# Optimization experiments

Measured on AMD Instinct MI355X. Metric: run time of the kernel, lower is better.

The kernel has to match this reference:

```python
import jax, jax.numpy as jnp
import numpy as np

N_NODES = 50000
N_EDGES = 800000
IN_CH, HID, OUT_CH, HEADS = 128, 32, 32, 8
NEG_SLOPE = 0.2


def setup_inputs() -> dict:
    key = jax.random.key(0)
    ks = jax.random.split(key, 20)
    x = jax.random.normal(ks[0], (N_NODES, IN_CH), dtype=jnp.float32)
    edge_index = jax.random.randint(ks[1], (2, N_EDGES), 0, N_NODES, dtype=jnp.int64)
    s = 0.1
    # encoder layer 1: in -> hid, heads=8 (concat)
    W1 = jax.random.normal(ks[2], (IN_CH, HEADS * HID), jnp.float32) * s
    as1 = jax.random.normal(ks[3], (HEADS, HID), jnp.float32) * s
    ad1 = jax.random.normal(ks[4], (HEADS, HID), jnp.float32) * s
    b1 = jnp.zeros((HEADS * HID,), jnp.float32)
    # encoder layer 2: hid*heads -> out, heads=1
    W2 = jax.random.normal(ks[5], (HEADS * HID, OUT_CH), jnp.float32) * s
    as2 = jax.random.normal(ks[6], (1, OUT_CH), jnp.float32) * s
    ad2 = jax.random.normal(ks[7], (1, OUT_CH), jnp.float32) * s
    b2 = jnp.zeros((OUT_CH,), jnp.float32)
    # decoder layer 1: out -> hid, heads=8 (concat)
    W3 = jax.random.normal(ks[8], (OUT_CH, HEADS * HID), jnp.float32) * s
    as3 = jax.random.normal(ks[9], (HEADS, HID), jnp.float32) * s
    ad3 = jax.random.normal(ks[10], (HEADS, HID), jnp.float32) * s
    b3 = jnp.zeros((HEADS * HID,), jnp.float32)
    # decoder layer 2: hid*heads -> in, heads=1
    W4 = jax.random.normal(ks[11], (HEADS * HID, IN_CH), jnp.float32) * s
    as4 = jax.random.normal(ks[12], (1, IN_CH), jnp.float32) * s
    ad4 = jax.random.normal(ks[13], (1, IN_CH), jnp.float32) * s
    b4 = jnp.zeros((IN_CH,), jnp.float32)
    return dict(x=x, edge_index=edge_index, W1=W1, as1=as1, ad1=ad1, b1=b1,
                W2=W2, as2=as2, ad2=ad2, b2=b2, W3=W3, as3=as3, ad3=ad3, b3=b3,
                W4=W4, as4=as4, ad4=ad4, b4=b4)


def gat_conv(x, src, dst, W, a_src, a_dst, b, heads, ch):
    # PyG GATConv: h = xW, e_ij = LeakyReLU(a_src.h_j + a_dst.h_i), softmax over incoming edges of i
    h = (x @ W).reshape(-1, heads, ch)                       # [N, H, C]
    al_s = jnp.sum(h * a_src[None], axis=-1)                 # [N, H]
    al_d = jnp.sum(h * a_dst[None], axis=-1)                 # [N, H]
    e = jax.nn.leaky_relu(al_s[src] + al_d[dst], NEG_SLOPE)  # [E, H]
    emax = jax.ops.segment_max(e, dst, num_segments=N_NODES)
    ee = jnp.exp(e - emax[dst])
    denom = jax.ops.segment_sum(ee, dst, num_segments=N_NODES)
    alpha = ee / denom[dst]                                  # [E, H]
    msg = alpha[:, :, None] * h[src]                         # [E, H, C]
    out = jax.ops.segment_sum(msg, dst, num_segments=N_NODES)  # [N, H, C]
    return out.reshape(N_NODES, heads * ch) + b


def reference(x, edge_index, W1, as1, ad1, b1, W2, as2, ad2, b2,
              W3, as3, ad3, b3, W4, as4, ad4, b4):
    # add self loops (PyG default add_self_loops=True)
    loop = jnp.arange(N_NODES, dtype=edge_index.dtype)
    src = jnp.concatenate([edge_index[0], loop])
    dst = jnp.concatenate([edge_index[1], loop])
    # encode
    z = gat_conv(x, src, dst, W1, as1, ad1, b1, HEADS, HID)
    z = jax.nn.relu(z)
    z = gat_conv(z, src, dst, W2, as2, ad2, b2, 1, OUT_CH)
    # decode
    r = gat_conv(z, src, dst, W3, as3, ad3, b3, HEADS, HID)
    r = jax.nn.relu(r)
    r = gat_conv(r, src, dst, W4, as4, ad4, b4, 1, IN_CH)
    return r
```

## Files before the change

kernel.cpp:

```cpp
#include <hip/hip_runtime.h>
#include <math.h>

#define N_NODES 50000
#define N_EDGES 800000
#define N_TOT   850000
#define NSB     ((N_NODES + 255) / 256)

typedef __attribute__((ext_vector_type(8))) short short8;
typedef __attribute__((ext_vector_type(4))) float floatx4;

__device__ __forceinline__ unsigned int pack_bf16x2(float a, float b) {
    unsigned ua = __float_as_uint(a);
    unsigned ub = __float_as_uint(b);
    ua += 0x7fff + ((ua >> 16) & 1);
    ub += 0x7fff + ((ub >> 16) & 1);
    return (ua >> 16) | (ub & 0xffff0000u);
}
__device__ __forceinline__ unsigned short pack_bf16(float a) {
    unsigned ua = __float_as_uint(a);
    ua += 0x7fff + ((ua >> 16) & 1);
    return (unsigned short)(ua >> 16);
}
__device__ __forceinline__ float bf16_lo(unsigned u) { return __uint_as_float(u << 16); }
__device__ __forceinline__ float bf16_hi(unsigned u) { return __uint_as_float(u & 0xffff0000u); }

__global__ void zero_int_kernel(int* p, int n) {
    int i = blockIdx.x * blockDim.x + threadIdx.x;
    if (i < n) p[i] = 0;
}

__global__ void deg_hist_kernel(const int* __restrict__ ei, int* __restrict__ deg) {
    int e = blockIdx.x * blockDim.x + threadIdx.x;
    if (e >= N_TOT) return;
    int dst = (e < N_EDGES) ? ei[N_EDGES + e] : (e - N_EDGES);
    atomicAdd(&deg[dst], 1);
}

__global__ void block_scan_kernel(const int* __restrict__ deg, int* __restrict__ part,
                                  int* __restrict__ bsum) {
    __shared__ int tmp[256];
    int t = threadIdx.x;
    int i = blockIdx.x * 256 + t;
    int v = (i < N_NODES) ? deg[i] : 0;
    tmp[t] = v;
    __syncthreads();
    for (int d = 1; d < 256; d <<= 1) {
        int u = (t >= d) ? tmp[t - d] : 0;
        __syncthreads();
        tmp[t] += u;
        __syncthreads();
    }
    if (i < N_NODES) part[i] = tmp[t] - v;
    if (t == 255) bsum[blockIdx.x] = tmp[255];
}

__global__ void scan_bsum_kernel(int* __restrict__ bsum) {
    __shared__ int tmp[256];
    int t = threadIdx.x;
    int v = (t < NSB) ? bsum[t] : 0;
    tmp[t] = v;
    __syncthreads();
    for (int d = 1; d < 256; d <<= 1) {
        int u = (t >= d) ? tmp[t - d] : 0;
        __syncthreads();
        tmp[t] += u;
        __syncthreads();
    }
    if (t < NSB) bsum[t] = tmp[t] - v;
}

__global__ void finalize_off_kernel(const int* __restrict__ part, const int* __restrict__ bsum,
                                    int* __restrict__ off, int* __restrict__ cursor) {
    int i = blockIdx.x * 256 + threadIdx.x;
    if (i < N_NODES) {
        int o = part[i] + bsum[blockIdx.x];
        off[i] = o;
        cursor[i] = o;
    }
    if (i == 0) off[N_NODES] = N_TOT;
}

__global__ void fill_csr_kernel(const int* __restrict__ ei, int* __restrict__ cursor,
                                int* __restrict__ csr_src) {
    int e = blockIdx.x * blockDim.x + threadIdx.x;
    if (e >= N_TOT) return;
    int src, dst;
    if (e < N_EDGES) { src = ei[e]; dst = ei[N_EDGES + e]; }
    else             { src = dst = e - N_EDGES; }
    int pos = atomicAdd(&cursor[dst], 1);
    csr_src[pos] = src;
}

__global__ void wconv_kernel(const float* __restrict__ W1, const float* __restrict__ W2,
                             const float* __restrict__ W3, const float* __restrict__ W4,
                             unsigned short* __restrict__ T1, unsigned short* __restrict__ T2,
                             unsigned short* __restrict__ T3, unsigned short* __restrict__ T4) {
    int i = blockIdx.x * 256 + threadIdx.x;
    const float* W; unsigned short* T; int K, N, idx;
    if      (i < 32768) { W = W1; T = T1; K = 128; N = 256; idx = i; }
    else if (i < 40960) { W = W2; T = T2; K = 256; N = 32;  idx = i - 32768; }
    else if (i < 49152) { W = W3; T = T3; K = 32;  N = 256; idx = i - 40960; }
    else if (i < 81920) { W = W4; T = T4; K = 256; N = 128; idx = i - 49152; }
    else return;
    int n = idx / K, k = idx % K;
    T[idx] = pack_bf16(W[(size_t)k * N + n]);
}

template<int Cin, int Cout, int H, int C, int NPB, int NW_N, bool IN_BF16>
__global__ void gemm_mfma_kernel(const void* __restrict__ xin,
                                 const unsigned short* __restrict__ Wt,
                                 const float* __restrict__ a_src, const float* __restrict__ a_dst,
                                 unsigned short* __restrict__ hb,
                                 float* __restrict__ al_s, float* __restrict__ al_d) {
    constexpr int NW_M = 4 / NW_N;
    constexpr int MT_W = (NPB / 16) / NW_M;
    constexpr int NT_W = (Cout / 16) / NW_N;
    constexpr int AS   = Cin + 8;
    constexpr int SP   = Cout + 4;
    __shared__ unsigned short xs[NPB * AS];
    __shared__ float hs[NPB * SP];
    int tid = threadIdx.x;
    int n0  = blockIdx.x * NPB;

    if (IN_BF16) {
        for (int i = tid; i < NPB * Cin / 8; i += 256) {
            int n = i / (Cin / 8), k8 = i % (Cin / 8);
            uint4 q = make_uint4(0u, 0u, 0u, 0u);
            if (n0 + n < N_NODES)
                q = ((const uint4*)((const unsigned short*)xin + (size_t)(n0 + n) * Cin))[k8];
            *(uint4*)(xs + n * AS + k8 * 8) = q;
        }
    } else {
        for (int i = tid; i < NPB * Cin / 4; i += 256) {
            int n = i / (Cin / 4), k4 = i % (Cin / 4);
            float4 v = make_float4(0.f, 0.f, 0.f, 0.f);
            if (n0 + n < N_NODES)
                v = ((const float4*)((const float*)xin + (size_t)(n0 + n) * Cin))[k4];
            uint2 p;
            p.x = pack_bf16x2(v.x, v.y);
            p.y = pack_bf16x2(v.z, v.w);
            *(uint2*)(xs + n * AS + k4 * 4) = p;
        }
    }
    __syncthreads();

    int w = tid >> 6, lane = tid & 63;
    int q = lane >> 4, l16 = lane & 15;
    int wm = w / NW_N, wn = w % NW_N;
    int mbase = wm * MT_W * 16;
    int nbase = wn * NT_W * 16;

    floatx4 acc[MT_W][NT_W];
#pragma unroll
    for (int mt = 0; mt < MT_W; mt++)
#pragma unroll
        for (int nt = 0; nt < NT_W; nt++) acc[mt][nt] = (floatx4){0.f, 0.f, 0.f, 0.f};

#pragma unroll
    for (int k0 = 0; k0 < Cin; k0 += 32) {
        short8 a[MT_W], b[NT_W];
#pragma unroll
        for (int mt = 0; mt < MT_W; mt++)
            a[mt] = *(const short8*)(xs + (mbase + mt * 16 + l16) * AS + k0 + q * 8);
#pragma unroll
        for (int nt = 0; nt < NT_W; nt++)
            b[nt] = *(const short8*)(Wt + (size_t)(nbase + nt * 16 + l16) * Cin + k0 + q * 8);
#pragma unroll
        for (int mt = 0; mt < MT_W; mt++)
#pragma unroll
            for (int nt = 0; nt < NT_W; nt++)
                acc[mt][nt] = __builtin_amdgcn_mfma_f32_16x16x32_bf16(a[mt], b[nt], acc[mt][nt], 0, 0, 0);
    }

#pragma unroll
    for (int mt = 0; mt < MT_W; mt++)
#pragma unroll
        for (int nt = 0; nt < NT_W; nt++)
#pragma unroll
            for (int r = 0; r < 4; r++) {
                int nl = mbase + mt * 16 + q * 4 + r;
                int ch = nbase + nt * 16 + l16;
                hs[nl * SP + ch] = acc[mt][nt][r];
            }
    __syncthreads();

    constexpr int TPN = Cout / 32;
    constexpr int TPH = (C > 32) ? (C / 32) : 1;
    if (tid < NPB * TPN) {
        int node = tid / TPN, sub = tid % TPN;
        int gn = n0 + node;
        int head = (sub * 32) / C;
        int coff = (sub * 32) % C;
        const float* hrow = hs + node * SP + sub * 32;
        const float* ap = a_src + head * C + coff;
        const float* dp = a_dst + head * C + coff;
        float ps = 0.f, pd = 0.f;
        unsigned pk[8];
#pragma unroll
        for (int c4 = 0; c4 < 8; c4++) {
            float4 hv = *(const float4*)(hrow + c4 * 4);
            float4 av = *(const float4*)(ap + c4 * 4);
            float4 dv = *(const float4*)(dp + c4 * 4);
            ps += hv.x * av.x + hv.y * av.y + hv.z * av.z + hv.w * av.w;
            pd += hv.x * dv.x + hv.y * dv.y + hv.z * dv.z + hv.w * dv.w;
            pk[c4] = pack_bf16x2(hv.x, hv.y) | 0u;
            pk[c4] = pack_bf16x2(hv.x, hv.y);
        }
        uint4 o0, o1;
        {
            float4 h0 = *(const float4*)(hrow + 0);
            float4 h1 = *(const float4*)(hrow + 4);
            float4 h2 = *(const float4*)(hrow + 8);
            float4 h3 = *(const float4*)(hrow + 12);
            o0.x = pack_bf16x2(h0.x, h0.y); o0.y = pack_bf16x2(h0.z, h0.w);
            o0.z = pack_bf16x2(h1.x, h1.y); o0.w = pack_bf16x2(h1.z, h1.w);
            o1.x = pack_bf16x2(h2.x, h2.y); o1.y = pack_bf16x2(h2.z, h2.w);
            o1.z = pack_bf16x2(h3.x, h3.y); o1.w = pack_bf16x2(h3.z, h3.w);
        }
        uint4 o2, o3;
        {
            float4 h0 = *(const float4*)(hrow + 16);
            float4 h1 = *(const float4*)(hrow + 20);
            float4 h2 = *(const float4*)(hrow + 24);
            float4 h3 = *(const float4*)(hrow + 28);
            o2.x = pack_bf16x2(h0.x, h0.y); o2.y = pack_bf16x2(h0.z, h0.w);
            o2.z = pack_bf16x2(h1.x, h1.y); o2.w = pack_bf16x2(h1.z, h1.w);
            o3.x = pack_bf16x2(h2.x, h2.y); o3.y = pack_bf16x2(h2.z, h2.w);
            o3.z = pack_bf16x2(h3.x, h3.y); o3.w = pack_bf16x2(h3.z, h3.w);
        }
        if (gn < N_NODES) {
            uint2* dst = (uint2*)(hb + (size_t)gn * Cout + sub * 32);
            dst[0] = make_uint2(o0.x, o0.y); dst[1] = make_uint2(o0.z, o0.w);
            dst[2] = make_uint2(o1.x, o1.y); dst[3] = make_uint2(o1.z, o1.w);
            dst[4] = make_uint2(o2.x, o2.y); dst[5] = make_uint2(o2.z, o2.w);
            dst[6] = make_uint2(o3.x, o3.y); dst[7] = make_uint2(o3.z, o3.w);
        }
        if (TPH > 1) {
#pragma unroll
            for (int k = 1; k < TPH; k <<= 1) {
                ps += __shfl_xor(ps, k, 64);
                pd += __shfl_xor(pd, k, 64);
            }
            if ((sub % TPH) == 0 && gn < N_NODES) {
                al_s[gn * H + head] = ps;
                al_d[gn * H + head] = pd;
            }
        } else {
            if (gn < N_NODES) {
                al_s[gn * H + head] = ps;
                al_d[gn * H + head] = pd;
            }
        }
    }
}

template<int H, int C, bool RELU, bool OUT_BF16>
__launch_bounds__(256, 8)
__global__ void gat_agg_kernel(const unsigned short* __restrict__ hb,
                               const float* __restrict__ al_s,
                               const float* __restrict__ al_d, const int* __restrict__ off,
                               const int* __restrict__ csr_src, const float* __restrict__ bias,
                               void* __restrict__ out) {
    constexpr int HC  = H * C;
    constexpr int G   = HC / 4;
    constexpr int SUB = G / H;
    constexpr int NPW = 64 / G;
    constexpr int NPB = 4 * NPW;

    int tid  = threadIdx.x;
    int wid  = tid >> 6;
    int lane = tid & 63;
    int gi   = lane / G;
    int g    = lane % G;
    int node = blockIdx.x * NPB + wid * NPW + gi;
    if (node >= N_NODES) return;

    int head = g / SUB;
    int es   = g % SUB;
    int r0 = off[node], r1 = off[node + 1];
    float ald = al_d[node * H + head];

    float m = -INFINITY, s = 0.f;
    for (int j = r0 + es; j < r1; j += SUB) {
        int src = csr_src[j];
        float e = al_s[src * H + head] + ald;
        e = (e > 0.f) ? e : 0.2f * e;
        float M = fmaxf(m, e);
        s = s * __expf(m - M) + __expf(e - M);
        m = M;
    }
#pragma unroll
    for (int k = 1; k < SUB; k <<= 1) {
        float om = __shfl_xor(m, k, 64);
        float os = __shfl_xor(s, k, 64);
        float M = fmaxf(m, om);
        float S;
        if (M == -INFINITY) S = 0.f;
        else S = s * __expf(m - M) + os * __expf(om - M);
        m = M; s = S;
    }
    float inv_s = 1.f / s;

    const uint2* hb2 = (const uint2*)hb;
    float4 acc = ((const float4*)bias)[g];
    int j0 = r0;
    for (; j0 + 8 <= r1; j0 += 8) {
        int srcs[8];
#pragma unroll
        for (int u = 0; u < 8; u++) srcs[u] = csr_src[j0 + u];
#pragma unroll
        for (int u = 0; u < 8; u++) {
            float e = al_s[srcs[u] * H + head] + ald;
            e = (e > 0.f) ? e : 0.2f * e;
            float we = __expf(e - m) * inv_s;
            uint2 q = hb2[(size_t)srcs[u] * (HC / 4) + g];
            acc.x += we * bf16_lo(q.x); acc.y += we * bf16_hi(q.x);
            acc.z += we * bf16_lo(q.y); acc.w += we * bf16_hi(q.y);
        }
    }
    for (; j0 < r1; j0++) {
        int src = csr_src[j0];
        float e = al_s[src * H + head] + ald;
        e = (e > 0.f) ? e : 0.2f * e;
        float we = __expf(e - m) * inv_s;
        uint2 q = hb2[(size_t)src * (HC / 4) + g];
        acc.x += we * bf16_lo(q.x); acc.y += we * bf16_hi(q.x);
        acc.z += we * bf16_lo(q.y); acc.w += we * bf16_hi(q.y);
    }
    if (RELU) {
        acc.x = fmaxf(acc.x, 0.f); acc.y = fmaxf(acc.y, 0.f);
        acc.z = fmaxf(acc.z, 0.f); acc.w = fmaxf(acc.w, 0.f);
    }
    if (OUT_BF16) {
        uint2 p;
        p.x = pack_bf16x2(acc.x, acc.y);
        p.y = pack_bf16x2(acc.z, acc.w);
        ((uint2*)out)[(size_t)node * (HC / 4) + g] = p;
    } else {
        ((float4*)out)[(size_t)node * (HC / 4) + g] = acc;
    }
}

extern "C" void kernel_launch(void* const* d_in, const int* in_sizes, int n_in,
                              void* d_out, int out_size, void* d_ws, size_t ws_size,
                              hipStream_t stream) {
    const float* x   = (const float*)d_in[0];
    const int*   ei  = (const int*)d_in[1];
    const float* W1  = (const float*)d_in[2];
    const float* as1 = (const float*)d_in[3];
    const float* ad1 = (const float*)d_in[4];
    const float* b1  = (const float*)d_in[5];
    const float* W2  = (const float*)d_in[6];
    const float* as2 = (const float*)d_in[7];
    const float* ad2 = (const float*)d_in[8];
    const float* b2  = (const float*)d_in[9];
    const float* W3  = (const float*)d_in[10];
    const float* as3 = (const float*)d_in[11];
    const float* ad3 = (const float*)d_in[12];
    const float* b3  = (const float*)d_in[13];
    const float* W4  = (const float*)d_in[14];
    const float* as4 = (const float*)d_in[15];
    const float* ad4 = (const float*)d_in[16];
    const float* b4  = (const float*)d_in[17];

    char* ws = (char*)d_ws;
    size_t o = 0;
    auto alloc = [&](size_t bytes) -> void* {
        void* p = ws + o;
        o = (o + bytes + 255) & ~(size_t)255;
        return p;
    };
    unsigned short* feat_a  = (unsigned short*)alloc((size_t)N_NODES * 256 * 2);
    unsigned short* feat_b  = (unsigned short*)alloc((size_t)N_NODES * 32 * 2);
    unsigned short* h_buf   = (unsigned short*)alloc((size_t)N_NODES * 256 * 2);
    float*          al_s    = (float*)alloc((size_t)N_NODES * 8 * 4);
    float*          al_d    = (float*)alloc((size_t)N_NODES * 8 * 4);
    int*            deg     = (int*)alloc((size_t)(N_NODES + 1) * 4);
    int*            off     = (int*)alloc((size_t)(N_NODES + 1) * 4);
    int*            cursor  = (int*)alloc((size_t)N_NODES * 4);
    int*            part    = (int*)alloc((size_t)N_NODES * 4);
    int*            bsum    = (int*)alloc((size_t)256 * 4);
    int*            csr_src = (int*)alloc((size_t)N_TOT * 4);
    unsigned short* w1t     = (unsigned short*)alloc(32768 * 2);
    unsigned short* w2t     = (unsigned short*)alloc(8192 * 2);
    unsigned short* w3t     = (unsigned short*)alloc(8192 * 2);
    unsigned short* w4t     = (unsigned short*)alloc(32768 * 2);

    const int TPB = 256;
    int nb_nodes = (N_NODES + TPB - 1) / TPB;
    int nb_edges = (N_TOT + TPB - 1) / TPB;

    zero_int_kernel<<<nb_nodes, TPB, 0, stream>>>(deg, N_NODES);
    wconv_kernel<<<320, TPB, 0, stream>>>(W1, W2, W3, W4, w1t, w2t, w3t, w4t);
    deg_hist_kernel<<<nb_edges, TPB, 0, stream>>>(ei, deg);
    block_scan_kernel<<<NSB, TPB, 0, stream>>>(deg, part, bsum);
    scan_bsum_kernel<<<1, TPB, 0, stream>>>(bsum);
    finalize_off_kernel<<<NSB, TPB, 0, stream>>>(part, bsum, off, cursor);
    fill_csr_kernel<<<nb_edges, TPB, 0, stream>>>(ei, cursor, csr_src);

    auto agg_blocks = [](int hc) { return (N_NODES * (hc / 4) + 255) / 256; };

    gemm_mfma_kernel<128, 256, 8, 32, 32, 4, false>
        <<<(N_NODES + 31) / 32, TPB, 0, stream>>>(x, w1t, as1, ad1, h_buf, al_s, al_d);
    gat_agg_kernel<8, 32, true, true><<<agg_blocks(256), TPB, 0, stream>>>(h_buf, al_s, al_d, off, csr_src, b1, feat_a);

    gemm_mfma_kernel<256, 32, 1, 32, 64, 2, true>
        <<<(N_NODES + 63) / 64, TPB, 0, stream>>>(feat_a, w2t, as2, ad2, h_buf, al_s, al_d);
    gat_agg_kernel<1, 32, false, true><<<agg_blocks(32), TPB, 0, stream>>>(h_buf, al_s, al_d, off, csr_src, b2, feat_b);

    gemm_mfma_kernel<32, 256, 8, 32, 32, 4, true>
        <<<(N_NODES + 31) / 32, TPB, 0, stream>>>(feat_b, w3t, as3, ad3, h_buf, al_s, al_d);
    gat_agg_kernel<8, 32, true, true><<<agg_blocks(256), TPB, 0, stream>>>(h_buf, al_s, al_d, off, csr_src, b3, feat_a);

    gemm_mfma_kernel<256, 128, 1, 128, 32, 4, true>
        <<<(N_NODES + 31) / 32, TPB, 0, stream>>>(feat_a, w4t, as4, ad4, h_buf, al_s, al_d);
    gat_agg_kernel<1, 128, false, false><<<agg_blocks(128), TPB, 0, stream>>>(h_buf, al_s, al_d, off, csr_src, b4, d_out);
}
```

Before: 541.9 us.

## Widen aggregation gathers to 16 bytes and stage GEMM output as bf16 in shared memory

The aggregation kernel now has each thread handle 8 channels and load them with 16-byte uint4 gathers instead of 8-byte uint2, which halves the thread count per node and the number of gather instructions. The GEMM epilogue packs accumulators to bf16 straight into a shared buffer that aliases the input tile, cutting LDS use and allowing higher occupancy. Attention logits are now computed from the bf16-rounded values, which slightly changes numerics. Fewer threads per node in aggregation also lowers the parallelism available to hide gather latency.

```diff
diff --git a/kernel.cpp b/kernel.cpp
--- a/kernel.cpp
+++ b/kernel.cpp
@@ -116,9 +116,11 @@
     constexpr int MT_W = (NPB / 16) / NW_M;
     constexpr int NT_W = (Cout / 16) / NW_N;
     constexpr int AS   = Cin + 8;
-    constexpr int SP   = Cout + 4;
-    __shared__ unsigned short xs[NPB * AS];
-    __shared__ float hs[NPB * SP];
+    constexpr int HS   = Cout + 8;
+    constexpr size_t SMEM_EL = (size_t)NPB * ((AS > HS) ? AS : HS);
+    __shared__ uint4 smem_raw[(SMEM_EL * 2 + 15) / 16];
+    unsigned short* xs  = (unsigned short*)smem_raw;
+    unsigned short* hsb = (unsigned short*)smem_raw;
     int tid = threadIdx.x;
     int n0  = blockIdx.x * NPB;
 
@@ -171,6 +173,7 @@
             for (int nt = 0; nt < NT_W; nt++)
                 acc[mt][nt] = __builtin_amdgcn_mfma_f32_16x16x32_bf16(a[mt], b[nt], acc[mt][nt], 0, 0, 0);
     }
+    __syncthreads();
 
 #pragma unroll
     for (int mt = 0; mt < MT_W; mt++)
@@ -180,60 +183,41 @@
             for (int r = 0; r < 4; r++) {
                 int nl = mbase + mt * 16 + q * 4 + r;
                 int ch = nbase + nt * 16 + l16;
-                hs[nl * SP + ch] = acc[mt][nt][r];
+                hsb[nl * HS + ch] = pack_bf16(acc[mt][nt][r]);
             }
     __syncthreads();
 
-    constexpr int TPN = Cout / 32;
-    constexpr int TPH = (C > 32) ? (C / 32) : 1;
-    if (tid < NPB * TPN) {
-        int node = tid / TPN, sub = tid % TPN;
-        int gn = n0 + node;
-        int head = (sub * 32) / C;
-        int coff = (sub * 32) % C;
-        const float* hrow = hs + node * SP + sub * 32;
-        const float* ap = a_src + head * C + coff;
-        const float* dp = a_dst + head * C + coff;
+    constexpr int TPN = Cout / 16;
+    constexpr int TPH = C / 16;
+    for (int t = tid; t < NPB * TPN; t += 256) {
+        int nodeL = t / TPN, sub = t % TPN;
+        int gn = n0 + nodeL;
+        uint4 qv = *(const uint4*)(hsb + nodeL * HS + sub * 16);
+        int head = (sub * 16) / C;
+        int coff = (sub * 16) % C;
+        const float4* ap = (const float4*)(a_src + head * C + coff);
+        const float4* dp = (const float4*)(a_dst + head * C + coff);
+        float hv[16];
+        hv[0] = bf16_lo(qv.x); hv[1] = bf16_hi(qv.x);
+        hv[2] = bf16_lo(qv.y); hv[3] = bf16_hi(qv.y);
+        hv[4] = bf16_lo(qv.z); hv[5] = bf16_hi(qv.z);
+        hv[6] = bf16_lo(qv.w); hv[7] = bf16_hi(qv.w);
+        uint4 qv2 = *(const uint4*)(hsb + nodeL * HS + sub * 16 + 8);
+        hv[8]  = bf16_lo(qv2.x); hv[9]  = bf16_hi(qv2.x);
+        hv[10] = bf16_lo(qv2.y); hv[11] = bf16_hi(qv2.y);
+        hv[12] = bf16_lo(qv2.z); hv[13] = bf16_hi(qv2.z);
+        hv[14] = bf16_lo(qv2.w); hv[15] = bf16_hi(qv2.w);
         float ps = 0.f, pd = 0.f;
-        unsigned pk[8];
-#pragma unroll
-        for (int c4 = 0; c4 < 8; c4++) {
-            float4 hv = *(const float4*)(hrow + c4 * 4);
-            float4 av = *(const float4*)(ap + c4 * 4);
-            float4 dv = *(const float4*)(dp + c4 * 4);
-            ps += hv.x * av.x + hv.y * av.y + hv.z * av.z + hv.w * av.w;
-            pd += hv.x * dv.x + hv.y * dv.y + hv.z * dv.z + hv.w * dv.w;
-            pk[c4] = pack_bf16x2(hv.x, hv.y) | 0u;
-            pk[c4] = pack_bf16x2(hv.x, hv.y);
-        }
-        uint4 o0, o1;
-        {
-            float4 h0 = *(const float4*)(hrow + 0);
-            float4 h1 = *(const float4*)(hrow + 4);
-            float4 h2 = *(const float4*)(hrow + 8);
-            float4 h3 = *(const float4*)(hrow + 12);
-            o0.x = pack_bf16x2(h0.x, h0.y); o0.y = pack_bf16x2(h0.z, h0.w);
-            o0.z = pack_bf16x2(h1.x, h1.y); o0.w = pack_bf16x2(h1.z, h1.w);
-            o1.x = pack_bf16x2(h2.x, h2.y); o1.y = pack_bf16x2(h2.z, h2.w);
-            o1.z = pack_bf16x2(h3.x, h3.y); o1.w = pack_bf16x2(h3.z, h3.w);
-        }
-        uint4 o2, o3;
-        {
-            float4 h0 = *(const float4*)(hrow + 16);
-            float4 h1 = *(const float4*)(hrow + 20);
-            float4 h2 = *(const float4*)(hrow + 24);
-            float4 h3 = *(const float4*)(hrow + 28);
-            o2.x = pack_bf16x2(h0.x, h0.y); o2.y = pack_bf16x2(h0.z, h0.w);
-            o2.z = pack_bf16x2(h1.x, h1.y); o2.w = pack_bf16x2(h1.z, h1.w);
-            o3.x = pack_bf16x2(h2.x, h2.y); o3.y = pack_bf16x2(h2.z, h2.w);
-            o3.z = pack_bf16x2(h3.x, h3.y); o3.w = pack_bf16x2(h3.z, h3.w);
+#pragma unroll
+        for (int c4 = 0; c4 < 4; c4++) {
+            float4 av = ap[c4], dv = dp[c4];
+            ps += hv[c4*4+0]*av.x + hv[c4*4+1]*av.y + hv[c4*4+2]*av.z + hv[c4*4+3]*av.w;
+            pd += hv[c4*4+0]*dv.x + hv[c4*4+1]*dv.y + hv[c4*4+2]*dv.z + hv[c4*4+3]*dv.w;
         }
         if (gn < N_NODES) {
-            uint2* dst = (uint2*)(hb + (size_t)gn * Cout + sub * 32);
-            dst[0] = make_uint2(o0.x, o0.y); dst[1] = make_uint2(o0.z, o0.w);
-            dst[2] = make_uint2(o1.x, o1.y); dst[3] = make_uint2(o1.z, o1.w);
-            dst[4] = make_uint2(o2.x, o2.y); dst[5] = make_uint2(o2.z, o2.w);
-            dst[6] = make_uint2(o3.x, o3.y); dst[7] = make_uint2(o3.z, o3.w);
+            uint4* dst = (uint4*)(hb + (size_t)gn * Cout);
+            dst[sub * 2]     = qv;
+            dst[sub * 2 + 1] = qv2;
         }
         if (TPH > 1) {
 #pragma unroll
@@ -241,15 +225,10 @@
                 ps += __shfl_xor(ps, k, 64);
                 pd += __shfl_xor(pd, k, 64);
             }
-            if ((sub % TPH) == 0 && gn < N_NODES) {
-                al_s[gn * H + head] = ps;
-                al_d[gn * H + head] = pd;
-            }
-        } else {
-            if (gn < N_NODES) {
-                al_s[gn * H + head] = ps;
-                al_d[gn * H + head] = pd;
-            }
+        }
+        if ((sub % TPH) == 0 && gn < N_NODES) {
+            al_s[gn * H + head] = ps;
+            al_d[gn * H + head] = pd;
         }
     }
 }
@@ -262,8 +241,8 @@
                                const int* __restrict__ csr_src, const float* __restrict__ bias,
                                void* __restrict__ out) {
     constexpr int HC  = H * C;
-    constexpr int G   = HC / 4;
-    constexpr int SUB = G / H;
+    constexpr int G   = HC / 8;
+    constexpr int SUB = C / 8;
     constexpr int NPW = 64 / G;
     constexpr int NPB = 4 * NPW;
 
@@ -301,8 +280,14 @@
     }
     float inv_s = 1.f / s;
 
-    const uint2* hb2 = (const uint2*)hb;
-    float4 acc = ((const float4*)bias)[g];
+    const uint4* hb4 = (const uint4*)hb;
+    float a0, a1, a2, a3, a4, a5, a6, a7;
+    {
+        const float4* bp = (const float4*)(bias + 8 * g);
+        float4 b0 = bp[0], b1 = bp[1];
+        a0 = b0.x; a1 = b0.y; a2 = b0.z; a3 = b0.w;
+        a4 = b1.x; a5 = b1.y; a6 = b1.z; a7 = b1.w;
+    }
     int j0 = r0;
     for (; j0 + 8 <= r1; j0 += 8) {
         int srcs[8];
@@ -313,9 +298,11 @@
             float e = al_s[srcs[u] * H + head] + ald;
             e = (e > 0.f) ? e : 0.2f * e;
             float we = __expf(e - m) * inv_s;
-            uint2 q = hb2[(size_t)srcs[u] * (HC / 4) + g];
-            acc.x += we * bf16_lo(q.x); acc.y += we * bf16_hi(q.x);
-            acc.z += we * bf16_lo(q.y); acc.w += we * bf16_hi(q.y);
+            uint4 qv = hb4[(size_t)srcs[u] * G + g];
+            a0 += we * bf16_lo(qv.x); a1 += we * bf16_hi(qv.x);
+            a2 += we * bf16_lo(qv.y); a3 += we * bf16_hi(qv.y);
+            a4 += we * bf16_lo(qv.z); a5 += we * bf16_hi(qv.z);
+            a6 += we * bf16_lo(qv.w); a7 += we * bf16_hi(qv.w);
         }
     }
     for (; j0 < r1; j0++) {
@@ -323,21 +310,25 @@
         float e = al_s[src * H + head] + ald;
         e = (e > 0.f) ? e : 0.2f * e;
         float we = __expf(e - m) * inv_s;
-        uint2 q = hb2[(size_t)src * (HC / 4) + g];
-        acc.x += we * bf16_lo(q.x); acc.y += we * bf16_hi(q.x);
-        acc.z += we * bf16_lo(q.y); acc.w += we * bf16_hi(q.y);
+        uint4 qv = hb4[(size_t)src * G + g];
+        a0 += we * bf16_lo(qv.x); a1 += we * bf16_hi(qv.x);
+        a2 += we * bf16_lo(qv.y); a3 += we * bf16_hi(qv.y);
+        a4 += we * bf16_lo(qv.z); a5 += we * bf16_hi(qv.z);
+        a6 += we * bf16_lo(qv.w); a7 += we * bf16_hi(qv.w);
     }
     if (RELU) {
-        acc.x = fmaxf(acc.x, 0.f); acc.y = fmaxf(acc.y, 0.f);
-        acc.z = fmaxf(acc.z, 0.f); acc.w = fmaxf(acc.w, 0.f);
+        a0 = fmaxf(a0, 0.f); a1 = fmaxf(a1, 0.f); a2 = fmaxf(a2, 0.f); a3 = fmaxf(a3, 0.f);
+        a4 = fmaxf(a4, 0.f); a5 = fmaxf(a5, 0.f); a6 = fmaxf(a6, 0.f); a7 = fmaxf(a7, 0.f);
     }
     if (OUT_BF16) {
-        uint2 p;
-        p.x = pack_bf16x2(acc.x, acc.y);
-        p.y = pack_bf16x2(acc.z, acc.w);
-        ((uint2*)out)[(size_t)node * (HC / 4) + g] = p;
+        uint4 p;
+        p.x = pack_bf16x2(a0, a1); p.y = pack_bf16x2(a2, a3);
+        p.z = pack_bf16x2(a4, a5); p.w = pack_bf16x2(a6, a7);
+        ((uint4*)out)[(size_t)node * G + g] = p;
     } else {
-        ((float4*)out)[(size_t)node * (HC / 4) + g] = acc;
+        float4* op = (float4*)out + (size_t)node * (HC / 4) + 2 * g;
+        op[0] = make_float4(a0, a1, a2, a3);
+        op[1] = make_float4(a4, a5, a6, a7);
     }
 }
 
@@ -398,7 +389,7 @@
     finalize_off_kernel<<<NSB, TPB, 0, stream>>>(part, bsum, off, cursor);
     fill_csr_kernel<<<nb_edges, TPB, 0, stream>>>(ei, cursor, csr_src);
 
-    auto agg_blocks = [](int hc) { return (N_NODES * (hc / 4) + 255) / 256; };
+    auto agg_blocks = [](int hc) { return (N_NODES * (hc / 8) + 255) / 256; };
 
     gemm_mfma_kernel<128, 256, 8, 32, 32, 4, false>
         <<<(N_NODES + 31) / 32, TPB, 0, stream>>>(x, w1t, as1, ad1, h_buf, al_s, al_d);
```

Result: slower. 733.1 us (+35.3%).
